# Kernel optimization log

Hardware: AMD Instinct MI355X
Metric: run time of the kernel (lower is better)

The kernel has to match this reference:

```python
import jax, jax.numpy as jnp
import numpy as np

N, E, F_IN, H, L = 1536, 49152, 27, 64, 32


def _ln(x, g, b, eps=1e-5):
    m = x.mean(-1, keepdims=True)
    v = ((x - m) ** 2).mean(-1, keepdims=True)
    return (x - m) * jax.lax.rsqrt(v + eps) * g + b


def _gatv2(x, src, dst, Wl, bl, Wr, br, att, bias, n):
    # PyG GATv2Conv, heads=1: alpha_ij = softmax_j( att . leaky_relu(Wl x_j + Wr x_i) )
    xl = x @ Wl + bl  # source transform [n,H]
    xr = x @ Wr + br  # target transform [n,H]
    e = jax.nn.leaky_relu(xl[src] + xr[dst], 0.2)  # [E',H]
    s = e @ att  # [E'] attention logits
    m = jax.ops.segment_max(s, dst, num_segments=n)
    w = jnp.exp(s - m[dst])
    denom = jax.ops.segment_sum(w, dst, num_segments=n)
    alpha = w / denom[dst]
    return jax.ops.segment_sum(alpha[:, None] * xl[src], dst, num_segments=n) + bias


def _model(x, eps_nodes, eps_graph, edge_index,
           Wl1, bl1, Wr1, br1, att1, bias1,
           Wl2, bl2, Wr2, br2, att2, bias2,
           Wnm, bnm, Wnv, bnv, Wgm, bgm, Wgv, bgv,
           Wd1, bd1, ln1_g, ln1_b, Wd2, bd2, ln2_g, ln2_b, Wd3, bd3,
           We1, be1, lne_g, lne_b, We2, be2,
           Wf1, bf1, lnf_g, lnf_b, Wf2, bf2):
    n = x.shape[0]
    loop = jnp.arange(n)
    src = jnp.concatenate([edge_index[0], loop])  # add self loops (PyG default)
    dst = jnp.concatenate([edge_index[1], loop])
    h = jax.nn.relu(_gatv2(x, src, dst, Wl1, bl1, Wr1, br1, att1, bias1, n))
    h = jax.nn.relu(_gatv2(h, src, dst, Wl2, bl2, Wr2, br2, att2, bias2, n))
    node_mu = h @ Wnm + bnm
    node_logvar = h @ Wnv + bnv
    gh = h.mean(0)
    graph_mu = gh @ Wgm + bgm
    graph_logvar = gh @ Wgv + bgv
    z = node_mu + eps_nodes * jnp.exp(0.5 * node_logvar)  # node reparam (training)
    _zg = graph_mu + eps_graph * jnp.exp(0.5 * graph_logvar)  # z_graph: computed, unused downstream as in source
    # dec_node_features MLP
    nf = _ln(jax.nn.relu(z @ Wd1 + bd1), ln1_g, ln1_b)
    nf = _ln(jax.nn.relu(nf @ Wd2 + bd2), ln2_g, ln2_b)
    nf = nf @ Wd3 + bd3  # [n, F_IN]
    # feature_refinement (node_embeddings = h is passed in forward)
    nf = _ln(jax.nn.relu(jnp.concatenate([nf, h], -1) @ Wf1 + bf1), lnf_g, lnf_b)
    node_features = nf @ Wf2 + bf2
    # edge_pred over all i<j pairs, vectorized (replaces the O(N^2) python loop)
    iu, ju = jnp.triu_indices(n, k=1)
    ei = jnp.concatenate([z[iu], z[ju]], -1)  # [P, 2L]
    eh = _ln(jax.nn.relu(ei @ We1 + be1), lne_g, lne_b)
    edge_logits = (eh @ We2 + be2)[:, 0]  # [P]
    return node_features, edge_logits, node_mu, node_logvar, graph_mu, graph_logvar


def setup_inputs() -> dict:
    key = jax.random.key(0)
    ki = iter(jax.random.split(key, 40))
    def W(fi, fo):
        return jax.random.normal(next(ki), (fi, fo), jnp.float32) / np.sqrt(fi)
    z64 = jnp.zeros((H,), jnp.float32)
    o64 = jnp.ones((H,), jnp.float32)
    zL = jnp.zeros((L,), jnp.float32)
    zF = jnp.zeros((F_IN,), jnp.float32)
    inp = {}
    inp["x"] = jax.random.normal(next(ki), (N, F_IN), jnp.float32)
    inp["edge_index"] = jax.random.randint(next(ki), (2, E), 0, N)
    inp["eps_nodes"] = jax.random.normal(next(ki), (N, L), jnp.float32)
    inp["eps_graph"] = jax.random.normal(next(ki), (L,), jnp.float32)
    inp.update(Wl1=W(F_IN, H), bl1=z64, Wr1=W(F_IN, H), br1=z64,
               att1=jax.random.normal(next(ki), (H,), jnp.float32) / np.sqrt(H), bias1=z64,
               Wl2=W(H, H), bl2=z64, Wr2=W(H, H), br2=z64,
               att2=jax.random.normal(next(ki), (H,), jnp.float32) / np.sqrt(H), bias2=z64)
    inp.update(Wnm=W(H, L), bnm=zL, Wnv=W(H, L), bnv=zL,
               Wgm=W(H, L), bgm=zL, Wgv=W(H, L), bgv=zL)
    inp.update(Wd1=W(L, H), bd1=z64, ln1_g=o64, ln1_b=z64,
               Wd2=W(H, H), bd2=z64, ln2_g=o64, ln2_b=z64,
               Wd3=W(H, F_IN), bd3=zF)
    inp.update(We1=W(2 * L, H), be1=z64, lne_g=o64, lne_b=z64,
               We2=W(H, 1), be2=jnp.zeros((1,), jnp.float32))
    inp.update(Wf1=W(F_IN + H, H), bf1=z64, lnf_g=o64, lnf_b=z64,
               Wf2=W(H, F_IN), bf2=zF)
    return inp


def reference(x, edge_index, eps_nodes, eps_graph,
              Wl1, bl1, Wr1, br1, att1, bias1,
              Wl2, bl2, Wr2, br2, att2, bias2,
              Wnm, bnm, Wnv, bnv, Wgm, bgm, Wgv, bgv,
              Wd1, bd1, ln1_g, ln1_b, Wd2, bd2, ln2_g, ln2_b, Wd3, bd3,
              We1, be1, lne_g, lne_b, We2, be2,
              Wf1, bf1, lnf_g, lnf_b, Wf2, bf2):
    return _model(x, eps_nodes, eps_graph, edge_index,
                  Wl1, bl1, Wr1, br1, att1, bias1,
                  Wl2, bl2, Wr2, br2, att2, bias2,
                  Wnm, bnm, Wnv, bnv, Wgm, bgm, Wgv, bgv,
                  Wd1, bd1, ln1_g, ln1_b, Wd2, bd2, ln2_g, ln2_b, Wd3, bd3,
                  We1, be1, lne_g, lne_b, We2, be2,
                  Wf1, bf1, lnf_g, lnf_b, Wf2, bf2)
```

## Files before the change

### kernel.cpp

```cpp
#include <hip/hip_runtime.h>

#define NN 1536
#define NE 49152
#define NM (NE + NN)
#define FIN 27
#define HD 64
#define LDIM 32
#define PP 1178880

#define EL_OFF  (NN*FIN)
#define MU_OFF  (EL_OFF + PP)
#define LV_OFF  (MU_OFF + NN*LDIM)
#define GMU_OFF (LV_OFF + NN*LDIM)
#define GLV_OFF (GMU_OFF + LDIM)

__device__ __forceinline__ float wsum(float v) {
#pragma unroll
  for (int m = 1; m < 64; m <<= 1) v += __shfl_xor(v, m, 64);
  return v;
}
__device__ __forceinline__ void wsum2(float& a, float& b) {
#pragma unroll
  for (int m = 1; m < 64; m <<= 1) {
    a += __shfl_xor(a, m, 64);
    b += __shfl_xor(b, m, 64);
  }
}
__device__ __forceinline__ float lnorm64(float x, float g, float b) {
  float s1 = x, s2 = x * x;
  wsum2(s1, s2);
  float mu = s1 * (1.0f / 64.0f);
  float var = fmaf(-mu, mu, s2 * (1.0f / 64.0f));
  return (x - mu) * rsqrtf(var + 1e-5f) * g + b;
}
__device__ __forceinline__ void cp4(float* dst, const float* __restrict__ src,
                                    int n4, int t) {
  const float4* s4 = (const float4*)src;
  float4* d4 = (float4*)dst;
  for (int e = t; e < n4; e += 256) d4[e] = s4[e];
}

__device__ __forceinline__ float gat_gather(const int* __restrict__ rowptr,
                                            const int* __restrict__ slot,
                                            const float* __restrict__ xl,
                                            float xri, float ak, int i, int k) {
  int beg = rowptr[i], end = rowptr[i + 1];
  float acc = 0.f, den = 0.f;
  for (int e0 = beg; e0 < end; e0 += 64) {
    int sidx = (e0 + k < end) ? slot[e0 + k] : 0;
    int nn = min(64, end - e0);
    int j = 0;
    for (; j + 1 < nn; j += 2) {
      int s0 = __shfl(sidx, j, 64), s1 = __shfl(sidx, j + 1, 64);
      float x0 = xl[s0 * HD + k], x1 = xl[s1 * HD + k];
      float e0v = x0 + xri, e1v = x1 + xri;
      e0v = fmaxf(e0v, 0.2f * e0v);
      e1v = fmaxf(e1v, 0.2f * e1v);
      float p0 = e0v * ak, p1 = e1v * ak;
      wsum2(p0, p1);
      float w0 = expf(p0), w1 = expf(p1);
      acc = fmaf(w0, x0, acc); den += w0;
      acc = fmaf(w1, x1, acc); den += w1;
    }
    if (j < nn) {
      int s0 = __shfl(sidx, j, 64);
      float x0 = xl[s0 * HD + k];
      float e0v = x0 + xri;
      e0v = fmaxf(e0v, 0.2f * e0v);
      float w0 = expf(wsum(e0v * ak));
      acc = fmaf(w0, x0, acc); den += w0;
    }
  }
  return acc / den;
}

__global__ __launch_bounds__(256) void gvae_xform1(
    const float* __restrict__ in,
    const float* __restrict__ Wl, const float* __restrict__ bl,
    const float* __restrict__ Wr, const float* __restrict__ br,
    float* __restrict__ xl, float* __restrict__ xr,
    const int* __restrict__ ei, int* __restrict__ cnt) {
  __shared__ __align__(16) float sWl[FIN * HD];
  __shared__ __align__(16) float sWr[FIN * HD];
  int t = threadIdx.x;
  int gid = blockIdx.x * 256 + t;
  if (gid < NE) atomicAdd(&cnt[ei[NE + gid]], 1);
  cp4(sWl, Wl, FIN * 16, t);
  cp4(sWr, Wr, FIN * 16, t);
  int i = blockIdx.x * 4 + (t >> 6);
  int k = t & 63;
  float xv = (k < FIN) ? in[i * FIN + k] : 0.f;
  float l0 = bl[k], l1 = 0.f, r0 = br[k], r1 = 0.f;
  __syncthreads();
#pragma unroll
  for (int a = 0; a < FIN; a += 2) {
    float xa = __shfl(xv, a, 64);
    l0 = fmaf(xa, sWl[a * HD + k], l0);
    r0 = fmaf(xa, sWr[a * HD + k], r0);
    if (a + 1 < FIN) {
      float xb = __shfl(xv, a + 1, 64);
      l1 = fmaf(xb, sWl[(a + 1) * HD + k], l1);
      r1 = fmaf(xb, sWr[(a + 1) * HD + k], r1);
    }
  }
  xl[i * HD + k] = l0 + l1;
  xr[i * HD + k] = r0 + r1;
}

__global__ __launch_bounds__(256) void gvae_scan(
    const int* __restrict__ cnt, int* __restrict__ rowptr,
    int* __restrict__ cursor, int* __restrict__ slot) {
  __shared__ int part[256];
  int t = threadIdx.x;
  int base = t * 6;
  int v[6];
  int s = 0;
#pragma unroll
  for (int j = 0; j < 6; j++) { v[j] = cnt[base + j] + 1; s += v[j]; }
  part[t] = s;
  __syncthreads();
  for (int off = 1; off < 256; off <<= 1) {
    int y = (t >= off) ? part[t - off] : 0;
    __syncthreads();
    part[t] += y;
    __syncthreads();
  }
  int r = part[t] - s;
#pragma unroll
  for (int j = 0; j < 6; j++) {
    int node = base + j;
    rowptr[node] = r;
    slot[r] = node;
    cursor[node] = r + 1;
    r += v[j];
  }
  if (t == 255) rowptr[NN] = r;
}

__global__ __launch_bounds__(256) void gvae_scatter(
    const int* __restrict__ ei, int* __restrict__ cursor, int* __restrict__ slot) {
  int m = blockIdx.x * 256 + threadIdx.x;
  if (m < NE) {
    int d = ei[NE + m];
    int p = atomicAdd(&cursor[d], 1);
    slot[p] = ei[m];
  }
}

__global__ __launch_bounds__(256) void gvae_gatherx(
    const int* __restrict__ rowptr, const int* __restrict__ slot,
    const float* __restrict__ xl, const float* __restrict__ xr,
    const float* __restrict__ att, const float* __restrict__ hbias,
    const float* __restrict__ Wl, const float* __restrict__ bl,
    const float* __restrict__ Wr, const float* __restrict__ br,
    float* __restrict__ xlo, float* __restrict__ xro) {
  __shared__ __align__(16) float sWl[HD * HD];
  __shared__ __align__(16) float sWr[HD * HD];
  int t = threadIdx.x;
  cp4(sWl, Wl, HD * 16, t);
  cp4(sWr, Wr, HD * 16, t);
  int i = blockIdx.x * 4 + (t >> 6);
  int k = t & 63;
  float xri = xr[i * HD + k];
  float ak = att[k];
  float hv = fmaxf(gat_gather(rowptr, slot, xl, xri, ak, i, k) + hbias[k], 0.f);
  float l0 = bl[k], l1 = 0.f, r0 = br[k], r1 = 0.f;
  __syncthreads();
#pragma unroll
  for (int a = 0; a < HD; a += 2) {
    float xa = __shfl(hv, a, 64);
    float xb = __shfl(hv, a + 1, 64);
    l0 = fmaf(xa, sWl[a * HD + k], l0);
    r0 = fmaf(xa, sWr[a * HD + k], r0);
    l1 = fmaf(xb, sWl[(a + 1) * HD + k], l1);
    r1 = fmaf(xb, sWr[(a + 1) * HD + k], r1);
  }
  xlo[i * HD + k] = l0 + l1;
  xro[i * HD + k] = r0 + r1;
}

#define oE1 0
#define oD1 4096
#define oD2 6144
#define oF1 10240
#define SWTOT 16064

__global__ __launch_bounds__(256, 2) void gvae_node(
    const int* __restrict__ rowptr, const int* __restrict__ slot,
    const float* __restrict__ xl, const float* __restrict__ xr,
    const float* __restrict__ att, const float* __restrict__ bias2,
    const float* __restrict__ eps,
    const float* __restrict__ Wnm, const float* __restrict__ bnm,
    const float* __restrict__ Wnv, const float* __restrict__ bnv,
    const float* __restrict__ We1, const float* __restrict__ be1,
    const float* __restrict__ Wd1, const float* __restrict__ bd1,
    const float* __restrict__ g1, const float* __restrict__ b1,
    const float* __restrict__ Wd2, const float* __restrict__ bd2,
    const float* __restrict__ g2, const float* __restrict__ b2,
    const float* __restrict__ Wd3, const float* __restrict__ bd3,
    const float* __restrict__ Wf1, const float* __restrict__ bf1,
    const float* __restrict__ gf, const float* __restrict__ bfv,
    const float* __restrict__ Wf2, const float* __restrict__ bf2,
    float* __restrict__ uo, float* __restrict__ vo,
    float* __restrict__ gh, float* __restrict__ out) {
  __shared__ __align__(16) float sW[SWTOT];
  __shared__ float ghred[256];
  int t = threadIdx.x;
  cp4(sW + oE1, We1, 1024, t);
  cp4(sW + oD1, Wd1, 512, t);
  cp4(sW + oD2, Wd2, 1024, t);
  cp4(sW + oF1, Wf1, 1456, t);

  int i = blockIdx.x * 4 + (t >> 6);
  int k = t & 63;
  int kk = k & 31;
  int kc = (k < FIN) ? k : (FIN - 1);

  float xri = xr[i * HD + k];
  float ak = att[k];
  float h2k = fmaxf(gat_gather(rowptr, slot, xl, xri, ak, i, k) + bias2[k], 0.f);
  ghred[t] = h2k;
  __syncthreads();
  if (t < 64) {
    float s = (ghred[t] + ghred[t + 64]) + (ghred[t + 128] + ghred[t + 192]);
    atomicAdd(&gh[t], s * (1.0f / NN));
  }

  const float* W = (k < 32) ? Wnm : Wnv;
  float c0 = (k < 32) ? bnm[kk] : bnv[kk];
  float c1 = 0.f, c2 = 0.f, c3 = 0.f;
#pragma unroll
  for (int a = 0; a < HD; a += 4) {
    c0 = fmaf(__shfl(h2k, a, 64),     W[a * LDIM + kk],       c0);
    c1 = fmaf(__shfl(h2k, a + 1, 64), W[(a + 1) * LDIM + kk], c1);
    c2 = fmaf(__shfl(h2k, a + 2, 64), W[(a + 2) * LDIM + kk], c2);
    c3 = fmaf(__shfl(h2k, a + 3, 64), W[(a + 3) * LDIM + kk], c3);
  }
  float acc = (c0 + c1) + (c2 + c3);
  if (k < 32) out[MU_OFF + i * LDIM + kk] = acc;
  else        out[LV_OFF + i * LDIM + kk] = acc;

  float lv = __shfl(acc, k + 32, 64);
  float zk = acc + eps[i * LDIM + kk] * expf(0.5f * lv);

  float u0 = be1[k], u1 = 0.f, v0 = 0.f, v1 = 0.f;
#pragma unroll
  for (int a = 0; a < LDIM; a += 2) {
    float za = __shfl(zk, a, 64);
    float zb = __shfl(zk, a + 1, 64);
    u0 = fmaf(za, sW[oE1 + a * HD + k], u0);
    u1 = fmaf(zb, sW[oE1 + (a + 1) * HD + k], u1);
    v0 = fmaf(za, sW[oE1 + (a + LDIM) * HD + k], v0);
    v1 = fmaf(zb, sW[oE1 + (a + 1 + LDIM) * HD + k], v1);
  }
  uo[i * HD + k] = u0 + u1;
  vo[i * HD + k] = v0 + v1;

  c0 = bd1[k]; c1 = 0.f; c2 = 0.f; c3 = 0.f;
#pragma unroll
  for (int a = 0; a < LDIM; a += 4) {
    c0 = fmaf(__shfl(zk, a, 64),     sW[oD1 + a * HD + k],       c0);
    c1 = fmaf(__shfl(zk, a + 1, 64), sW[oD1 + (a + 1) * HD + k], c1);
    c2 = fmaf(__shfl(zk, a + 2, 64), sW[oD1 + (a + 2) * HD + k], c2);
    c3 = fmaf(__shfl(zk, a + 3, 64), sW[oD1 + (a + 3) * HD + k], c3);
  }
  float nf1 = lnorm64(fmaxf((c0 + c1) + (c2 + c3), 0.f), g1[k], b1[k]);

  c0 = bd2[k]; c1 = 0.f; c2 = 0.f; c3 = 0.f;
#pragma unroll
  for (int a = 0; a < HD; a += 4) {
    c0 = fmaf(__shfl(nf1, a, 64),     sW[oD2 + a * HD + k],       c0);
    c1 = fmaf(__shfl(nf1, a + 1, 64), sW[oD2 + (a + 1) * HD + k], c1);
    c2 = fmaf(__shfl(nf1, a + 2, 64), sW[oD2 + (a + 2) * HD + k], c2);
    c3 = fmaf(__shfl(nf1, a + 3, 64), sW[oD2 + (a + 3) * HD + k], c3);
  }
  float nf2 = lnorm64(fmaxf((c0 + c1) + (c2 + c3), 0.f), g2[k], b2[k]);

  c0 = 0.f; c1 = 0.f; c2 = 0.f; c3 = 0.f;
#pragma unroll
  for (int a = 0; a < HD; a += 4) {
    c0 = fmaf(__shfl(nf2, a, 64),     Wd3[a * FIN + kc],       c0);
    c1 = fmaf(__shfl(nf2, a + 1, 64), Wd3[(a + 1) * FIN + kc], c1);
    c2 = fmaf(__shfl(nf2, a + 2, 64), Wd3[(a + 2) * FIN + kc], c2);
    c3 = fmaf(__shfl(nf2, a + 3, 64), Wd3[(a + 3) * FIN + kc], c3);
  }
  float nf3 = (k < FIN) ? ((c0 + c1) + (c2 + c3) + bd3[kc]) : 0.f;

  c0 = bf1[k]; c1 = 0.f; c2 = 0.f; c3 = 0.f;
#pragma unroll
  for (int j = 0; j < FIN; j++) {
    float nj = __shfl(nf3, j, 64);
    c0 = fmaf(nj, sW[oF1 + j * HD + k], c0);
  }
#pragma unroll
  for (int a = 0; a < HD; a += 4) {
    c0 = fmaf(__shfl(h2k, a, 64),     sW[oF1 + (FIN + a) * HD + k],     c0);
    c1 = fmaf(__shfl(h2k, a + 1, 64), sW[oF1 + (FIN + a + 1) * HD + k], c1);
    c2 = fmaf(__shfl(h2k, a + 2, 64), sW[oF1 + (FIN + a + 2) * HD + k], c2);
    c3 = fmaf(__shfl(h2k, a + 3, 64), sW[oF1 + (FIN + a + 3) * HD + k], c3);
  }
  float rr = lnorm64(fmaxf((c0 + c1) + (c2 + c3), 0.f), gf[k], bfv[k]);

  c0 = 0.f; c1 = 0.f; c2 = 0.f; c3 = 0.f;
#pragma unroll
  for (int a = 0; a < HD; a += 4) {
    c0 = fmaf(__shfl(rr, a, 64),     Wf2[a * FIN + kc],       c0);
    c1 = fmaf(__shfl(rr, a + 1, 64), Wf2[(a + 1) * FIN + kc], c1);
    c2 = fmaf(__shfl(rr, a + 2, 64), Wf2[(a + 2) * FIN + kc], c2);
    c3 = fmaf(__shfl(rr, a + 3, 64), Wf2[(a + 3) * FIN + kc], c3);
  }
  if (k < FIN) out[i * FIN + k] = (c0 + c1) + (c2 + c3) + bf2[kc];
}

__global__ __launch_bounds__(256) void gvae_edge(
    const float* __restrict__ u, const float* __restrict__ v,
    const float* __restrict__ lng, const float* __restrict__ lnb,
    const float* __restrict__ w2, const float* __restrict__ be2,
    const float* __restrict__ gh,
    const float* __restrict__ Wgm, const float* __restrict__ bgm,
    const float* __restrict__ Wgv, const float* __restrict__ bgv,
    float* __restrict__ out) {
  __shared__ float U[64 * 64];
  __shared__ float V[64 * 68];
  __shared__ float C[64];
  __shared__ float cc[2];
  int t = threadIdx.x;
  int wv = t >> 6, lane = t & 63;

  if (blockIdx.x == 0 && wv == 3) {
    int kk = lane & 31;
    float ghk = gh[lane];
    const float* W = (lane < 32) ? Wgm : Wgv;
    float c0 = (lane < 32) ? bgm[kk] : bgv[kk];
    float c1 = 0.f, c2 = 0.f, c3 = 0.f;
#pragma unroll
    for (int a = 0; a < HD; a += 4) {
      c0 = fmaf(__shfl(ghk, a, 64),     W[a * LDIM + kk],       c0);
      c1 = fmaf(__shfl(ghk, a + 1, 64), W[(a + 1) * LDIM + kk], c1);
      c2 = fmaf(__shfl(ghk, a + 2, 64), W[(a + 2) * LDIM + kk], c2);
      c3 = fmaf(__shfl(ghk, a + 3, 64), W[(a + 3) * LDIM + kk], c3);
    }
    float acc = (c0 + c1) + (c2 + c3);
    if (lane < 32) out[GMU_OFF + kk] = acc;
    else           out[GLV_OFF + kk] = acc;
  }

  int rem = blockIdx.x, bi = 0;
  while (rem >= 24 - bi) { rem -= 24 - bi; bi++; }
  int bj = bi + rem;

  const float4* u4p = (const float4*)(u + bi * 64 * HD);
  const float4* v4p = (const float4*)(v + bj * 64 * HD);
#pragma unroll
  for (int it = 0; it < 4; ++it) {
    int r = t + it * 256;
    int row = r >> 4, q = r & 15;
    float4 uu = u4p[r];
    *(float4*)&U[row * 64 + q * 4] = uu;
    float4 vvv = v4p[r];
    *(float4*)&V[row * 68 + q * 4] = vvv;
  }
  if (t < 64) {
    float ck = lng[t] * w2[t];
    C[t] = ck;
    float cb = lnb[t] * w2[t];
    float sC = wsum(ck);
    float sB = wsum(cb);
    if (t == 0) { cc[0] = sC; cc[1] = sB + be2[0]; }
  }
  __syncthreads();
  float C1 = cc[0], C0 = cc[1];

  float S1[16], S2[16], Sc[16];
#pragma unroll
  for (int ii = 0; ii < 16; ii++) { S1[ii] = 0.f; S2[ii] = 0.f; Sc[ii] = 0.f; }
  const float* Ub = &U[(wv * 16) * 64];
  for (int k4 = 0; k4 < 16; k4++) {
    float4 v4 = *(const float4*)&V[lane * 68 + k4 * 4];
    float4 c4 = *(const float4*)&C[k4 * 4];
#pragma unroll
    for (int ii = 0; ii < 16; ii++) {
      float4 u4 = *(const float4*)&Ub[ii * 64 + k4 * 4];
      float t0 = fmaxf(u4.x + v4.x, 0.f);
      float t1 = fmaxf(u4.y + v4.y, 0.f);
      float t2 = fmaxf(u4.z + v4.z, 0.f);
      float t3 = fmaxf(u4.w + v4.w, 0.f);
      S1[ii] += (t0 + t1) + (t2 + t3);
      S2[ii] = fmaf(t0, t0, fmaf(t1, t1, fmaf(t2, t2, fmaf(t3, t3, S2[ii]))));
      Sc[ii] = fmaf(t0, c4.x, fmaf(t1, c4.y, fmaf(t2, c4.z, fmaf(t3, c4.w, Sc[ii]))));
    }
  }
  int j = bj * 64 + lane;
  const float inv64 = 1.0f / 64.0f;
#pragma unroll
  for (int ii = 0; ii < 16; ii++) {
    int i = bi * 64 + wv * 16 + ii;
    if (j > i) {
      int pbase = i * (2 * NN - i - 1) / 2 - i - 1;
      float mu = S1[ii] * inv64;
      float var = fmaf(-mu, mu, S2[ii] * inv64);
      float logit = (Sc[ii] - mu * C1) * rsqrtf(var + 1e-5f) + C0;
      out[EL_OFF + pbase + j] = logit;
    }
  }
}

extern "C" void kernel_launch(void* const* d_in, const int* in_sizes, int n_in,
                              void* d_out, int out_size, void* d_ws, size_t ws_size,
                              hipStream_t stream) {
  const float* x    = (const float*)d_in[0];
  const int*   ei   = (const int*)d_in[1];
  const float* eps  = (const float*)d_in[2];
  const float* Wl1  = (const float*)d_in[4];
  const float* bl1  = (const float*)d_in[5];
  const float* Wr1  = (const float*)d_in[6];
  const float* br1  = (const float*)d_in[7];
  const float* att1 = (const float*)d_in[8];
  const float* bias1= (const float*)d_in[9];
  const float* Wl2  = (const float*)d_in[10];
  const float* bl2  = (const float*)d_in[11];
  const float* Wr2  = (const float*)d_in[12];
  const float* br2  = (const float*)d_in[13];
  const float* att2 = (const float*)d_in[14];
  const float* bias2= (const float*)d_in[15];
  const float* Wnm  = (const float*)d_in[16];
  const float* bnm  = (const float*)d_in[17];
  const float* Wnv  = (const float*)d_in[18];
  const float* bnv  = (const float*)d_in[19];
  const float* Wgm  = (const float*)d_in[20];
  const float* bgm  = (const float*)d_in[21];
  const float* Wgv  = (const float*)d_in[22];
  const float* bgv  = (const float*)d_in[23];
  const float* Wd1  = (const float*)d_in[24];
  const float* bd1  = (const float*)d_in[25];
  const float* ln1g = (const float*)d_in[26];
  const float* ln1b = (const float*)d_in[27];
  const float* Wd2  = (const float*)d_in[28];
  const float* bd2  = (const float*)d_in[29];
  const float* ln2g = (const float*)d_in[30];
  const float* ln2b = (const float*)d_in[31];
  const float* Wd3  = (const float*)d_in[32];
  const float* bd3  = (const float*)d_in[33];
  const float* We1  = (const float*)d_in[34];
  const float* be1  = (const float*)d_in[35];
  const float* lneg = (const float*)d_in[36];
  const float* lneb = (const float*)d_in[37];
  const float* We2  = (const float*)d_in[38];
  const float* be2  = (const float*)d_in[39];
  const float* Wf1  = (const float*)d_in[40];
  const float* bf1  = (const float*)d_in[41];
  const float* lnfg = (const float*)d_in[42];
  const float* lnfb = (const float*)d_in[43];
  const float* Wf2  = (const float*)d_in[44];
  const float* bf2  = (const float*)d_in[45];
  float* out = (float*)d_out;

  float* fb  = (float*)d_ws;
  float* xl1 = fb;
  float* xr1 = xl1 + NN * HD;
  float* xl2 = xr1 + NN * HD;
  float* xr2 = xl2 + NN * HD;
  float* uu  = xr2 + NN * HD;
  float* vv  = uu  + NN * HD;
  float* gh  = vv  + NN * HD;
  int* cnt    = (int*)(gh + HD);
  int* rowptr = cnt + NN;
  int* cursor = rowptr + NN + 1;
  int* slot   = cursor + NN;

  hipMemsetAsync(gh, 0, (HD + NN) * sizeof(float), stream);

  gvae_xform1<<<NN / 4, 256, 0, stream>>>(x, Wl1, bl1, Wr1, br1, xl1, xr1, ei, cnt);
  gvae_scan<<<1, 256, 0, stream>>>(cnt, rowptr, cursor, slot);
  gvae_scatter<<<NE / 256, 256, 0, stream>>>(ei, cursor, slot);
  gvae_gatherx<<<NN / 4, 256, 0, stream>>>(rowptr, slot, xl1, xr1, att1, bias1,
                                           Wl2, bl2, Wr2, br2, xl2, xr2);
  gvae_node<<<NN / 4, 256, 0, stream>>>(rowptr, slot, xl2, xr2, att2, bias2, eps,
      Wnm, bnm, Wnv, bnv, We1, be1,
      Wd1, bd1, ln1g, ln1b, Wd2, bd2, ln2g, ln2b, Wd3, bd3,
      Wf1, bf1, lnfg, lnfb, Wf2, bf2,
      uu, vv, gh, out);
  gvae_edge<<<300, 256, 0, stream>>>(uu, vv, lneg, lneb, We2, be2,
                                     gh, Wgm, bgm, Wgv, bgv, out);
}
```

Measured before the change: 242.2 us.

## Drop shared-memory weight staging in GAT and node kernels, widen gather unroll

Stops copying weight matrices into LDS in gvae_gatherx and gvae_node and reads them straight from global memory (L1/L2 cached), removing the copy and barrier and shrinking LDS so more blocks fit per CU. gvae_node's launch bounds go from 2 to 4 blocks per SM. The attention gather loop is unrolled by 4 with a four-way wave reduction to raise memory-level parallelism. The trade-off is uncached per-lane global loads of weights instead of LDS reads, plus higher register pressure from the wider unroll.

```diff
diff --git a/kernel.cpp b/kernel.cpp
--- a/kernel.cpp
+++ b/kernel.cpp
@@ -24,6 +24,15 @@
   for (int m = 1; m < 64; m <<= 1) {
     a += __shfl_xor(a, m, 64);
     b += __shfl_xor(b, m, 64);
+  }
+}
+__device__ __forceinline__ void wsum4(float& a, float& b, float& c, float& d) {
+#pragma unroll
+  for (int m = 1; m < 64; m <<= 1) {
+    a += __shfl_xor(a, m, 64);
+    b += __shfl_xor(b, m, 64);
+    c += __shfl_xor(c, m, 64);
+    d += __shfl_xor(d, m, 64);
   }
 }
 __device__ __forceinline__ float lnorm64(float x, float g, float b) {
@@ -50,19 +59,25 @@
     int sidx = (e0 + k < end) ? slot[e0 + k] : 0;
     int nn = min(64, end - e0);
     int j = 0;
-    for (; j + 1 < nn; j += 2) {
-      int s0 = __shfl(sidx, j, 64), s1 = __shfl(sidx, j + 1, 64);
+    for (; j + 3 < nn; j += 4) {
+      int s0 = __shfl(sidx, j, 64),     s1 = __shfl(sidx, j + 1, 64);
+      int s2 = __shfl(sidx, j + 2, 64), s3 = __shfl(sidx, j + 3, 64);
       float x0 = xl[s0 * HD + k], x1 = xl[s1 * HD + k];
-      float e0v = x0 + xri, e1v = x1 + xri;
+      float x2 = xl[s2 * HD + k], x3 = xl[s3 * HD + k];
+      float e0v = x0 + xri, e1v = x1 + xri, e2v = x2 + xri, e3v = x3 + xri;
       e0v = fmaxf(e0v, 0.2f * e0v);
       e1v = fmaxf(e1v, 0.2f * e1v);
-      float p0 = e0v * ak, p1 = e1v * ak;
-      wsum2(p0, p1);
-      float w0 = expf(p0), w1 = expf(p1);
+      e2v = fmaxf(e2v, 0.2f * e2v);
+      e3v = fmaxf(e3v, 0.2f * e3v);
+      float p0 = e0v * ak, p1 = e1v * ak, p2 = e2v * ak, p3 = e3v * ak;
+      wsum4(p0, p1, p2, p3);
+      float w0 = expf(p0), w1 = expf(p1), w2 = expf(p2), w3 = expf(p3);
       acc = fmaf(w0, x0, acc); den += w0;
       acc = fmaf(w1, x1, acc); den += w1;
-    }
-    if (j < nn) {
+      acc = fmaf(w2, x2, acc); den += w2;
+      acc = fmaf(w3, x3, acc); den += w3;
+    }
+    for (; j < nn; ++j) {
       int s0 = __shfl(sidx, j, 64);
       float x0 = xl[s0 * HD + k];
       float e0v = x0 + xri;
@@ -154,38 +169,27 @@
     const float* __restrict__ Wl, const float* __restrict__ bl,
     const float* __restrict__ Wr, const float* __restrict__ br,
     float* __restrict__ xlo, float* __restrict__ xro) {
-  __shared__ __align__(16) float sWl[HD * HD];
-  __shared__ __align__(16) float sWr[HD * HD];
   int t = threadIdx.x;
-  cp4(sWl, Wl, HD * 16, t);
-  cp4(sWr, Wr, HD * 16, t);
   int i = blockIdx.x * 4 + (t >> 6);
   int k = t & 63;
   float xri = xr[i * HD + k];
   float ak = att[k];
   float hv = fmaxf(gat_gather(rowptr, slot, xl, xri, ak, i, k) + hbias[k], 0.f);
   float l0 = bl[k], l1 = 0.f, r0 = br[k], r1 = 0.f;
-  __syncthreads();
 #pragma unroll
   for (int a = 0; a < HD; a += 2) {
     float xa = __shfl(hv, a, 64);
     float xb = __shfl(hv, a + 1, 64);
-    l0 = fmaf(xa, sWl[a * HD + k], l0);
-    r0 = fmaf(xa, sWr[a * HD + k], r0);
-    l1 = fmaf(xb, sWl[(a + 1) * HD + k], l1);
-    r1 = fmaf(xb, sWr[(a + 1) * HD + k], r1);
+    l0 = fmaf(xa, Wl[a * HD + k], l0);
+    r0 = fmaf(xa, Wr[a * HD + k], r0);
+    l1 = fmaf(xb, Wl[(a + 1) * HD + k], l1);
+    r1 = fmaf(xb, Wr[(a + 1) * HD + k], r1);
   }
   xlo[i * HD + k] = l0 + l1;
   xro[i * HD + k] = r0 + r1;
 }
 
-#define oE1 0
-#define oD1 4096
-#define oD2 6144
-#define oF1 10240
-#define SWTOT 16064
-
-__global__ __launch_bounds__(256, 2) void gvae_node(
+__global__ __launch_bounds__(256, 4) void gvae_node(
     const int* __restrict__ rowptr, const int* __restrict__ slot,
     const float* __restrict__ xl, const float* __restrict__ xr,
     const float* __restrict__ att, const float* __restrict__ bias2,
@@ -203,14 +207,8 @@
     const float* __restrict__ Wf2, const float* __restrict__ bf2,
     float* __restrict__ uo, float* __restrict__ vo,
     float* __restrict__ gh, float* __restrict__ out) {
-  __shared__ __align__(16) float sW[SWTOT];
   __shared__ float ghred[256];
   int t = threadIdx.x;
-  cp4(sW + oE1, We1, 1024, t);
-  cp4(sW + oD1, Wd1, 512, t);
-  cp4(sW + oD2, Wd2, 1024, t);
-  cp4(sW + oF1, Wf1, 1456, t);
-
   int i = blockIdx.x * 4 + (t >> 6);
   int k = t & 63;
   int kk = k & 31;
@@ -248,10 +246,10 @@
   for (int a = 0; a < LDIM; a += 2) {
     float za = __shfl(zk, a, 64);
     float zb = __shfl(zk, a + 1, 64);
-    u0 = fmaf(za, sW[oE1 + a * HD + k], u0);
-    u1 = fmaf(zb, sW[oE1 + (a + 1) * HD + k], u1);
-    v0 = fmaf(za, sW[oE1 + (a + LDIM) * HD + k], v0);
-    v1 = fmaf(zb, sW[oE1 + (a + 1 + LDIM) * HD + k], v1);
+    u0 = fmaf(za, We1[a * HD + k], u0);
+    u1 = fmaf(zb, We1[(a + 1) * HD + k], u1);
+    v0 = fmaf(za, We1[(a + LDIM) * HD + k], v0);
+    v1 = fmaf(zb, We1[(a + 1 + LDIM) * HD + k], v1);
   }
   uo[i * HD + k] = u0 + u1;
   vo[i * HD + k] = v0 + v1;
@@ -259,20 +257,20 @@
   c0 = bd1[k]; c1 = 0.f; c2 = 0.f; c3 = 0.f;
 #pragma unroll
   for (int a = 0; a < LDIM; a += 4) {
-    c0 = fmaf(__shfl(zk, a, 64),     sW[oD1 + a * HD + k],       c0);
-    c1 = fmaf(__shfl(zk, a + 1, 64), sW[oD1 + (a + 1) * HD + k], c1);
-    c2 = fmaf(__shfl(zk, a + 2, 64), sW[oD1 + (a + 2) * HD + k], c2);
-    c3 = fmaf(__shfl(zk, a + 3, 64), sW[oD1 + (a + 3) * HD + k], c3);
+    c0 = fmaf(__shfl(zk, a, 64),     Wd1[a * HD + k],       c0);
+    c1 = fmaf(__shfl(zk, a + 1, 64), Wd1[(a + 1) * HD + k], c1);
+    c2 = fmaf(__shfl(zk, a + 2, 64), Wd1[(a + 2) * HD + k], c2);
+    c3 = fmaf(__shfl(zk, a + 3, 64), Wd1[(a + 3) * HD + k], c3);
   }
   float nf1 = lnorm64(fmaxf((c0 + c1) + (c2 + c3), 0.f), g1[k], b1[k]);
 
   c0 = bd2[k]; c1 = 0.f; c2 = 0.f; c3 = 0.f;
 #pragma unroll
   for (int a = 0; a < HD; a += 4) {
-    c0 = fmaf(__shfl(nf1, a, 64),     sW[oD2 + a * HD + k],       c0);
-    c1 = fmaf(__shfl(nf1, a + 1, 64), sW[oD2 + (a + 1) * HD + k], c1);
-    c2 = fmaf(__shfl(nf1, a + 2, 64), sW[oD2 + (a + 2) * HD + k], c2);
-    c3 = fmaf(__shfl(nf1, a + 3, 64), sW[oD2 + (a + 3) * HD + k], c3);
+    c0 = fmaf(__shfl(nf1, a, 64),     Wd2[a * HD + k],       c0);
+    c1 = fmaf(__shfl(nf1, a + 1, 64), Wd2[(a + 1) * HD + k], c1);
+    c2 = fmaf(__shfl(nf1, a + 2, 64), Wd2[(a + 2) * HD + k], c2);
+    c3 = fmaf(__shfl(nf1, a + 3, 64), Wd2[(a + 3) * HD + k], c3);
   }
   float nf2 = lnorm64(fmaxf((c0 + c1) + (c2 + c3), 0.f), g2[k], b2[k]);
 
@@ -290,14 +288,14 @@
 #pragma unroll
   for (int j = 0; j < FIN; j++) {
     float nj = __shfl(nf3, j, 64);
-    c0 = fmaf(nj, sW[oF1 + j * HD + k], c0);
+    c0 = fmaf(nj, Wf1[j * HD + k], c0);
   }
 #pragma unroll
   for (int a = 0; a < HD; a += 4) {
-    c0 = fmaf(__shfl(h2k, a, 64),     sW[oF1 + (FIN + a) * HD + k],     c0);
-    c1 = fmaf(__shfl(h2k, a + 1, 64), sW[oF1 + (FIN + a + 1) * HD + k], c1);
-    c2 = fmaf(__shfl(h2k, a + 2, 64), sW[oF1 + (FIN + a + 2) * HD + k], c2);
-    c3 = fmaf(__shfl(h2k, a + 3, 64), sW[oF1 + (FIN + a + 3) * HD + k], c3);
+    c0 = fmaf(__shfl(h2k, a, 64),     Wf1[(FIN + a) * HD + k],     c0);
+    c1 = fmaf(__shfl(h2k, a + 1, 64), Wf1[(FIN + a + 1) * HD + k], c1);
+    c2 = fmaf(__shfl(h2k, a + 2, 64), Wf1[(FIN + a + 2) * HD + k], c2);
+    c3 = fmaf(__shfl(h2k, a + 3, 64), Wf1[(FIN + a + 3) * HD + k], c3);
   }
   float rr = lnorm64(fmaxf((c0 + c1) + (c2 + c3), 0.f), gf[k], bfv[k]);
 
@@ -357,8 +355,8 @@
     int row = r >> 4, q = r & 15;
     float4 uu = u4p[r];
     *(float4*)&U[row * 64 + q * 4] = uu;
-    float4 vvv = v4p[r];
-    *(float4*)&V[row * 68 + q * 4] = vvv;
+    float4 vv = v4p[r];
+    *(float4*)&V[row * 68 + q * 4] = vv;
   }
   if (t < 64) {
     float ck = lng[t] * w2[t];
```

After: 240.3 us. About the same (-0.8%).
